# Optimization experiments

Hardware: AMD Instinct MI355X
Metric: run time of the kernel (lower is better)

Reference implementation:

```python
import jax, jax.numpy as jnp
import numpy as np

B, D, H, OUT = 1024, 1024, 16, 1000
DH = D // H          # 64 per-head dim
S = 50               # 49 patches + class token
EPS = 1e-5


def sinusoidal_pos_emb(seq_len, d_model):
    pos = jnp.arange(seq_len, dtype=jnp.float32)[:, None]
    i = jnp.arange(d_model, dtype=jnp.float32)[None, :]
    even = jnp.sin(pos / jnp.power(10000.0, i / d_model))
    odd = jnp.cos(pos / jnp.power(10000.0, (i - 1.0) / d_model))
    return jnp.where((jnp.arange(d_model) % 2 == 0)[None, :], even, odd)


def layernorm(x, w, b):
    mu = jnp.mean(x, axis=-1, keepdims=True)
    var = jnp.mean(jnp.square(x - mu), axis=-1, keepdims=True)
    return (x - mu) / jnp.sqrt(var + EPS) * w + b


def setup_inputs() -> dict:
    key = jax.random.key(0)
    ks = jax.random.split(key, 16)
    s = 1.0 / np.sqrt(DH)
    return {
        "x": jax.random.normal(ks[0], (B, 1, 28, 28), dtype=jnp.float32),
        "cls_token": jax.random.normal(ks[1], (1, D), dtype=jnp.float32),
        "Wp": jax.random.normal(ks[2], (D, 16), dtype=jnp.float32) * 0.25,
        "ln1_w": jnp.ones((D,), jnp.float32),
        "ln1_b": jnp.zeros((D,), jnp.float32),
        "Wq": jax.random.uniform(ks[3], (H, DH, DH), jnp.float32, -s, s),
        "bq": jax.random.uniform(ks[4], (H, DH), jnp.float32, -s, s),
        "Wk": jax.random.uniform(ks[5], (H, DH, DH), jnp.float32, -s, s),
        "bk": jax.random.uniform(ks[6], (H, DH), jnp.float32, -s, s),
        "Wv": jax.random.uniform(ks[7], (H, DH, DH), jnp.float32, -s, s),
        "bv": jax.random.uniform(ks[8], (H, DH), jnp.float32, -s, s),
        "ln2_w": jnp.ones((D,), jnp.float32),
        "ln2_b": jnp.zeros((D,), jnp.float32),
        "Wm": jax.random.normal(ks[9], (D, D), jnp.float32) / np.sqrt(D),
        "bm": jnp.zeros((D,), jnp.float32),
        "Wh": jax.random.normal(ks[10], (OUT, D), jnp.float32) / np.sqrt(D),
        "bh": jnp.zeros((OUT,), jnp.float32),
    }


def reference(x, cls_token, Wp, ln1_w, ln1_b, Wq, bq, Wk, bk, Wv, bv,
              ln2_w, ln2_b, Wm, bm, Wh, bh):
    b = x.shape[0]
    # patchify: (B,1,28,28) -> (B,49,16)  (7x7 patches of 4x4)
    p = x.reshape(b, 1, 7, 4, 7, 4).transpose(0, 1, 2, 4, 3, 5).reshape(b, 49, 16)
    tok = jnp.einsum('bps,ds->bpd', p, Wp)               # (B,49,D), no bias
    tok = jnp.concatenate([jnp.broadcast_to(cls_token[None], (b, 1, D)), tok], axis=1)
    tok = tok + sinusoidal_pos_emb(S, D)[None]           # (B,50,D)

    # transformer block (faithful: scores scaled by sqrt(d_model), full D)
    n = layernorm(tok, ln1_w, ln1_b)
    xh = n.reshape(b, S, H, DH).transpose(0, 2, 1, 3)    # (B,H,S,DH)
    q = jnp.einsum('bhsd,hed->bhse', xh, Wq) + bq[None, :, None, :]
    k = jnp.einsum('bhsd,hed->bhse', xh, Wk) + bk[None, :, None, :]
    v = jnp.einsum('bhsd,hed->bhse', xh, Wv) + bv[None, :, None, :]
    scores = jax.nn.softmax(jnp.einsum('bhqd,bhkd->bhqk', q, k) * jnp.sqrt(jnp.float32(D)), axis=-1)
    attn = jnp.einsum('bhqk,bhkd->bhqd', scores, v)      # (B,H,S,DH)
    A = attn.transpose(0, 2, 1, 3).reshape(b, S, D)
    tok = tok + A
    tok = tok + layernorm(tok, ln2_w, ln2_b) @ Wm.T + bm

    # classification head on class token
    logits = tok[:, 0] @ Wh.T + bh
    return jax.nn.softmax(logits, axis=-1)
```

## Files before the change

kernel.cpp:

```cpp
#include <hip/hip_runtime.h>
#include <math.h>


#define EPS 1e-5f

__device__ __forceinline__ float warp_sum64(float v) {
    #pragma unroll
    for (int off = 32; off >= 1; off >>= 1) v += __shfl_xor(v, off, 64);
    return v;
}
__device__ __forceinline__ float warp_max64(float v) {
    #pragma unroll
    for (int off = 32; off >= 1; off >>= 1) v = fmaxf(v, __shfl_xor(v, off, 64));
    return v;
}

__device__ __forceinline__ float block_sum(float v, float* red) {
    v = warp_sum64(v);
    int lane = threadIdx.x & 63, w = threadIdx.x >> 6;
    if (lane == 0) red[w] = v;
    __syncthreads();
    int nw = blockDim.x >> 6;
    if (w == 0) {
        float x = (lane < nw) ? red[lane] : 0.f;
        x = warp_sum64(x);
        if (lane == 0) red[0] = x;
    }
    __syncthreads();
    float r = red[0];
    __syncthreads();
    return r;
}

__device__ __forceinline__ float block_max(float v, float* red) {
    v = warp_max64(v);
    int lane = threadIdx.x & 63, w = threadIdx.x >> 6;
    if (lane == 0) red[w] = v;
    __syncthreads();
    int nw = blockDim.x >> 6;
    if (w == 0) {
        float x = (lane < nw) ? red[lane] : -INFINITY;
        x = warp_max64(x);
        if (lane == 0) red[0] = x;
    }
    __syncthreads();
    float r = red[0];
    __syncthreads();
    return r;
}

__global__ __launch_bounds__(256) void k_pe(float* __restrict__ pe) {
    int s = blockIdx.x;
    for (int d = threadIdx.x; d < 1024; d += 256) {
        int di = d & ~1;
        float freq = expf(-((float)di * (1.0f / 1024.f)) * 9.210340371976184f);
        float arg = (float)s * freq;
        pe[s * 1024 + d] = (d & 1) ? cosf(arg) : sinf(arg);
    }
}

__global__ __launch_bounds__(256) void k_prep_a(
    const float* __restrict__ cls, const float* __restrict__ pe,
    const float* __restrict__ ln1w, const float* __restrict__ ln1b,
    const float* __restrict__ Wq, const float* __restrict__ bq,
    const float* __restrict__ Wk,
    float* __restrict__ tok0c, float* __restrict__ n0g,
    float* __restrict__ qlw,
    float* __restrict__ score0, float* __restrict__ kap, float* __restrict__ bet)
{
    __shared__ float red[8];
    __shared__ float n0s[1024], q0s[1024];
    __shared__ float partA[256], partK[256], partB[256];
    int t = threadIdx.x;
    int h = t >> 4;

    float tv[4];
    #pragma unroll
    for (int i = 0; i < 4; ++i) {
        int d = t * 4 + i;
        tv[i] = cls[d] + pe[d];
        tok0c[d] = tv[i];
    }
    float sum = block_sum(tv[0] + tv[1] + tv[2] + tv[3], red);
    float mu = sum * (1.f / 1024.f);
    float d2 = 0.f;
    #pragma unroll
    for (int i = 0; i < 4; ++i) { float dv = tv[i] - mu; d2 = fmaf(dv, dv, d2); }
    float var = block_sum(d2, red) * (1.f / 1024.f);
    float rstd = rsqrtf(var + EPS);
    #pragma unroll
    for (int i = 0; i < 4; ++i) {
        int d = t * 4 + i;
        float nv = (tv[i] - mu) * rstd * ln1w[d] + ln1b[d];
        n0s[d] = nv; n0g[d] = nv;
    }
    __syncthreads();

    #pragma unroll
    for (int i = 0; i < 4; ++i) {
        int e = t * 4 + i, el = e & 63;
        const float* wr = Wq + ((size_t)h << 12) + el * 64;
        float acc = bq[e];
        for (int dd = 0; dd < 64; ++dd) acc = fmaf(wr[dd], n0s[(h << 6) + dd], acc);
        q0s[e] = acc;
    }
    __syncthreads();

    float pA = 0.f, pK = 0.f, pB = 0.f;
    #pragma unroll
    for (int i = 0; i < 4; ++i) {
        int d = t * 4 + i, dl = d & 63;
        const float* wc = Wk + ((size_t)h << 12) + dl;
        float acc = 0.f;
        for (int ee = 0; ee < 64; ++ee) acc = fmaf(wc[ee * 64], q0s[(h << 6) + ee], acc);
        acc *= 32.0f;
        float ql = acc * ln1w[d];
        qlw[d] = ql;
        pA = fmaf(acc, n0s[d], pA);
        pK += ql;
        pB = fmaf(acc, ln1b[d], pB);
    }
    partA[t] = pA; partK[t] = pK; partB[t] = pB;
    __syncthreads();
    if (t < 16) {
        float sA = 0.f, sK = 0.f, sB = 0.f;
        #pragma unroll
        for (int i = 0; i < 16; ++i) {
            sA += partA[t * 16 + i]; sK += partK[t * 16 + i]; sB += partB[t * 16 + i];
        }
        score0[t] = sA; kap[t] = sK; bet[t] = sB;
    }
}

__global__ __launch_bounds__(256) void k_prep_b(
    const float* __restrict__ pe, const float* __restrict__ Wp,
    const float* __restrict__ qlw,
    float* __restrict__ pwt, float* __restrict__ pe2t,
    float* __restrict__ pemean, float* __restrict__ pesum,
    float* __restrict__ Gt, float* __restrict__ ut, float* __restrict__ gt)
{
    int blk = blockIdx.x, t = threadIdx.x;
    if (blk < 50) {
        __shared__ float red[8];
        __shared__ float pwbuf[256 * 16];
        __shared__ float psbuf[256];
        int s = blk;
        float pwp[16];
        #pragma unroll
        for (int j = 0; j < 16; ++j) pwp[j] = 0.f;
        float pep = 0.f, pe2p = 0.f, psp = 0.f;
        #pragma unroll
        for (int i = 0; i < 4; ++i) {
            int d = t * 4 + i;
            float e = pe[s * 1024 + d];
            pep += e; pe2p = fmaf(e, e, pe2p); psp = fmaf(qlw[d], e, psp);
            const float* wr = Wp + (size_t)d * 16;
            #pragma unroll
            for (int j = 0; j < 16; ++j) pwp[j] = fmaf(wr[j], e, pwp[j]);
        }
        #pragma unroll
        for (int j = 0; j < 16; ++j) pwbuf[t * 16 + j] = pwp[j];
        psbuf[t] = psp;
        float pes = block_sum(pep, red);
        float pe2s = block_sum(pe2p, red);
        if (t < 16) {
            float a = 0.f;
            for (int k = 0; k < 256; ++k) a += pwbuf[k * 16 + t];
            pwt[s * 16 + t] = a;
            float b = 0.f;
            #pragma unroll
            for (int k = 0; k < 16; ++k) b += psbuf[t * 16 + k];
            pesum[s * 16 + t] = b;
        }
        if (t == 0) { pe2t[s] = pe2s; pemean[s] = pes * (1.f / 1024.f); }
    } else if (blk == 50) {
        int j = t >> 4, k = t & 15;
        float a = 0.f;
        for (int d = 0; d < 1024; ++d)
            a = fmaf(Wp[(size_t)d * 16 + j], Wp[(size_t)d * 16 + k], a);
        Gt[j * 16 + k] = a;
        if (t < 16) {
            float ua = 0.f;
            for (int d = 0; d < 1024; ++d) ua += Wp[(size_t)d * 16 + t];
            ut[t] = ua * (1.f / 1024.f);
        }
    } else {
        int h = t >> 4, j = t & 15;
        float a = 0.f;
        for (int dl = 0; dl < 64; ++dl) {
            int d = h * 64 + dl;
            a = fmaf(qlw[d], Wp[(size_t)d * 16 + j], a);
        }
        gt[h * 16 + j] = a;
    }
}

__global__ __launch_bounds__(256) void k_fused(
    const float* __restrict__ x, const float* __restrict__ pe,
    const float* __restrict__ Wp,
    const float* __restrict__ ln1w, const float* __restrict__ ln1b,
    const float* __restrict__ Wv, const float* __restrict__ bv,
    const float* __restrict__ n0g, const float* __restrict__ score0,
    const float* __restrict__ kap, const float* __restrict__ bet,
    const float* __restrict__ Gt, const float* __restrict__ ut,
    const float* __restrict__ gt,
    const float* __restrict__ pwt, const float* __restrict__ pe2t,
    const float* __restrict__ pemean, const float* __restrict__ pesum,
    float* __restrict__ A0)
{
    __shared__ float Gs[256], gs[256];
    __shared__ float us[16], kaps[16], bets[16], s0s[16];
    __shared__ int   prc[50];
    __shared__ float xs[4][800];
    __shared__ float mus[4][52], rss[4][52];
    __shared__ float sc[4][16][52];
    __shared__ float wpat[4][16][17];
    __shared__ float wmus[4][16];
    __shared__ float csh[4][16][68];

    int t = threadIdx.x, w = t >> 6, lane = t & 63;
    int b = blockIdx.x * 4 + w;

    Gs[t] = Gt[t];
    gs[t] = gt[t];
    if (t < 16) { us[t] = ut[t]; kaps[t] = kap[t]; bets[t] = bet[t]; s0s[t] = score0[t]; }
    if (t >= 1 && t < 50) prc[t] = ((t - 1) / 7) * 112 + ((t - 1) % 7) * 4;
    for (int i = lane; i < 784; i += 64) xs[w][i] = x[b * 784 + i];
    __syncthreads();

    {
        int s = lane;
        if (s >= 1 && s < 50) {
            float p[16];
            int off = prc[s];
            #pragma unroll
            for (int j = 0; j < 16; ++j) p[j] = xs[w][off + (j >> 2) * 28 + (j & 3)];
            float mu = pemean[s];
            #pragma unroll
            for (int j = 0; j < 16; ++j) mu = fmaf(us[j], p[j], mu);
            float ssq = pe2t[s];
            #pragma unroll
            for (int j = 0; j < 16; ++j) {
                float gpj = 0.f;
                #pragma unroll
                for (int k = 0; k < 16; ++k) gpj = fmaf(Gs[j * 16 + k], p[k], gpj);
                ssq = fmaf(p[j], gpj, ssq);
            }
            const float* pwr = pwt + s * 16;
            #pragma unroll
            for (int j = 0; j < 16; ++j) ssq = fmaf(2.f * p[j], pwr[j], ssq);
            float var = ssq * (1.f / 1024.f) - mu * mu;
            float rsv = rsqrtf(var + EPS);
            mus[w][s] = mu; rss[w][s] = rsv;
            const float* pss = pesum + s * 16;
            #pragma unroll
            for (int h = 0; h < 16; ++h) {
                float gp = 0.f;
                #pragma unroll
                for (int j = 0; j < 16; ++j) gp = fmaf(gs[h * 16 + j], p[j], gp);
                sc[w][h][s] = rsv * (gp + pss[h] - mu * kaps[h]) + bets[h];
            }
        } else if (s == 50) {
            #pragma unroll
            for (int h = 0; h < 16; ++h) sc[w][h][0] = s0s[h];
        }
    }
    __syncthreads();

    int h = lane & 15, q = lane >> 4;
    {
        int sb = q * 13, se = (sb + 13 < 50) ? sb + 13 : 50;
        float mx = -1e30f;
        for (int ss = sb; ss < se; ++ss) mx = fmaxf(mx, sc[w][h][ss]);
        mx = fmaxf(mx, __shfl_xor(mx, 16, 64));
        mx = fmaxf(mx, __shfl_xor(mx, 32, 64));
        float sm = 0.f;
        for (int ss = sb; ss < se; ++ss) {
            float e = expf(sc[w][h][ss] - mx);
            sc[w][h][ss] = e;
            sm += e;
        }
        sm += __shfl_xor(sm, 16, 64);
        sm += __shfl_xor(sm, 32, 64);
        float inv = 1.f / sm;
        for (int ss = sb; ss < se; ++ss) sc[w][h][ss] *= inv;
    }
    __syncthreads();

    {
        int sb = q * 13, se = (sb + 13 < 50) ? sb + 13 : 50;
        int s0c = (q == 0) ? 1 : sb;
        float acc[16], amu = 0.f;
        #pragma unroll
        for (int j = 0; j < 16; ++j) acc[j] = 0.f;
        for (int ss = s0c; ss < se; ++ss) {
            float wgt = sc[w][h][ss] * rss[w][ss];
            int off = prc[ss];
            #pragma unroll
            for (int j = 0; j < 16; ++j)
                acc[j] = fmaf(wgt, xs[w][off + (j >> 2) * 28 + (j & 3)], acc[j]);
            amu = fmaf(wgt, mus[w][ss], amu);
        }
        #pragma unroll
        for (int j = 0; j < 16; ++j) {
            acc[j] += __shfl_xor(acc[j], 16, 64);
            acc[j] += __shfl_xor(acc[j], 32, 64);
        }
        amu += __shfl_xor(amu, 16, 64);
        amu += __shfl_xor(amu, 32, 64);
        if (q == 0) {
            #pragma unroll
            for (int j = 0; j < 16; ++j) wpat[w][h][j] = acc[j];
            wmus[w][h] = amu;
        }
    }
    __syncthreads();

    {
        int d0 = lane * 16;
        int hh = lane >> 2;
        int dl0 = (lane & 3) * 16;
        float p0 = sc[w][hh][0];
        float wpe[16];
        #pragma unroll
        for (int i = 0; i < 16; ++i) wpe[i] = 0.f;
        for (int ss = 1; ss < 50; ++ss) {
            float wgt = sc[w][hh][ss] * rss[w][ss];
            const float4* per = (const float4*)(pe + ss * 1024 + d0);
            #pragma unroll
            for (int i4 = 0; i4 < 4; ++i4) {
                float4 v = per[i4];
                wpe[i4 * 4 + 0] = fmaf(wgt, v.x, wpe[i4 * 4 + 0]);
                wpe[i4 * 4 + 1] = fmaf(wgt, v.y, wpe[i4 * 4 + 1]);
                wpe[i4 * 4 + 2] = fmaf(wgt, v.z, wpe[i4 * 4 + 2]);
                wpe[i4 * 4 + 3] = fmaf(wgt, v.w, wpe[i4 * 4 + 3]);
            }
        }
        float wmu = wmus[w][hh];
        #pragma unroll
        for (int i = 0; i < 16; ++i) {
            int d = d0 + i;
            const float* wr = Wp + (size_t)d * 16;
            float wp_ = 0.f;
            #pragma unroll
            for (int j = 0; j < 16; ++j) wp_ = fmaf(wr[j], wpat[w][hh][j], wp_);
            float ci = p0 * n0g[d] + ln1w[d] * (wp_ + wpe[i] - wmu)
                     + ln1b[d] * (1.f - p0);
            csh[w][hh][dl0 + i] = ci;
        }
    }
    __syncthreads();

    {
        int e0 = lane * 16;
        int hh = lane >> 2;
        int el0 = (lane & 3) * 16;
        #pragma unroll
        for (int i = 0; i < 16; ++i) {
            int e = e0 + i;
            const float* wr = Wv + ((size_t)hh << 12) + (el0 + i) * 64;
            float acc = bv[e];
            #pragma unroll 16
            for (int dd = 0; dd < 64; ++dd)
                acc = fmaf(wr[dd], csh[w][hh][dd], acc);
            A0[(size_t)b * 1024 + e] = acc;
        }
    }
}

__global__ __launch_bounds__(256) void k_c1(
    const float* __restrict__ tok0c, const float* __restrict__ A0,
    const float* __restrict__ w2, const float* __restrict__ b2,
    float* __restrict__ tok0, float* __restrict__ n2)
{
    int b = blockIdx.x, tid = threadIdx.x;
    __shared__ float red[8];
    float t[4];
    #pragma unroll
    for (int i = 0; i < 4; ++i) {
        int d = tid + (i << 8);
        t[i] = tok0c[d] + A0[(size_t)b * 1024 + d];
    }
    float sum = block_sum(t[0] + t[1] + t[2] + t[3], red);
    float mu = sum * (1.f / 1024.f);
    float d2 = 0.f;
    #pragma unroll
    for (int i = 0; i < 4; ++i) { float dv = t[i] - mu; d2 = fmaf(dv, dv, d2); }
    float var = block_sum(d2, red) * (1.f / 1024.f);
    float rstd = rsqrtf(var + EPS);
    #pragma unroll
    for (int i = 0; i < 4; ++i) {
        int d = tid + (i << 8);
        tok0[(size_t)b * 1024 + d] = t[i];
        n2[(size_t)b * 1024 + d] = (t[i] - mu) * rstd * w2[d] + b2[d];
    }
}

__global__ __launch_bounds__(256) void k_gemm_sk(
    const float* __restrict__ A, const float* __restrict__ Bw,
    float* __restrict__ Cp, int N, int K)
{
    __shared__ __align__(16) float As[32 * 68];
    __shared__ __align__(16) float Bs[32 * 68];
    int n0 = blockIdx.x * 64, m0 = blockIdx.y * 64;
    int kz = blockIdx.z;
    int tid = threadIdx.x;
    int mt = (tid & 15) * 4, nt = (tid >> 4) * 4;
    float acc[4][4] = {{0.f}};

    int kbeg = kz * 128;
    for (int k0 = kbeg; k0 < kbeg + 128; k0 += 32) {
        for (int idx = tid; idx < 64 * 32; idx += 256) {
            int kk = idx & 31, m = idx >> 5;
            As[kk * 68 + m] = A[(size_t)(m0 + m) * K + k0 + kk];
            float bvv = (n0 + m < N) ? Bw[(size_t)(n0 + m) * K + k0 + kk] : 0.f;
            Bs[kk * 68 + m] = bvv;
        }
        __syncthreads();
        #pragma unroll 8
        for (int kk = 0; kk < 32; ++kk) {
            float4 av = *(const float4*)&As[kk * 68 + mt];
            float4 bv = *(const float4*)&Bs[kk * 68 + nt];
            acc[0][0] = fmaf(av.x, bv.x, acc[0][0]);
            acc[0][1] = fmaf(av.x, bv.y, acc[0][1]);
            acc[0][2] = fmaf(av.x, bv.z, acc[0][2]);
            acc[0][3] = fmaf(av.x, bv.w, acc[0][3]);
            acc[1][0] = fmaf(av.y, bv.x, acc[1][0]);
            acc[1][1] = fmaf(av.y, bv.y, acc[1][1]);
            acc[1][2] = fmaf(av.y, bv.z, acc[1][2]);
            acc[1][3] = fmaf(av.y, bv.w, acc[1][3]);
            acc[2][0] = fmaf(av.z, bv.x, acc[2][0]);
            acc[2][1] = fmaf(av.z, bv.y, acc[2][1]);
            acc[2][2] = fmaf(av.z, bv.z, acc[2][2]);
            acc[2][3] = fmaf(av.z, bv.w, acc[2][3]);
            acc[3][0] = fmaf(av.w, bv.x, acc[3][0]);
            acc[3][1] = fmaf(av.w, bv.y, acc[3][1]);
            acc[3][2] = fmaf(av.w, bv.z, acc[3][2]);
            acc[3][3] = fmaf(av.w, bv.w, acc[3][3]);
        }
        __syncthreads();
    }

    float* cpb = Cp + (size_t)kz * ((size_t)1024 * N);
    #pragma unroll
    for (int i = 0; i < 4; ++i) {
        int r = m0 + mt + i;
        #pragma unroll
        for (int j = 0; j < 4; ++j) {
            int c = n0 + nt + j;
            if (c < N) cpb[(size_t)r * N + c] = acc[i][j];
        }
    }
}

__global__ __launch_bounds__(256) void k_reduce(
    const float* __restrict__ Cp, const float* __restrict__ bias,
    const float* __restrict__ res, float* __restrict__ C, int N)
{
    const int N4 = N >> 2;
    int e4 = blockIdx.x * 256 + threadIdx.x;
    if (e4 >= 1024 * N4) return;
    int r = e4 / N4;
    int c = (e4 - r * N4) << 2;
    size_t off = (size_t)r * N + c;
    const size_t slice = (size_t)1024 * N;
    float4 s = make_float4(0.f, 0.f, 0.f, 0.f);
    #pragma unroll
    for (int kz = 0; kz < 8; ++kz) {
        float4 v = *(const float4*)(Cp + kz * slice + off);
        s.x += v.x; s.y += v.y; s.z += v.z; s.w += v.w;
    }
    float4 bb = *(const float4*)(bias + c);
    s.x += bb.x; s.y += bb.y; s.z += bb.z; s.w += bb.w;
    if (res) {
        float4 rv = *(const float4*)(res + off);
        s.x += rv.x; s.y += rv.y; s.z += rv.z; s.w += rv.w;
    }
    *(float4*)(C + off) = s;
}

__global__ __launch_bounds__(256) void k_softmax(
    const float* __restrict__ logits, float* __restrict__ out)
{
    int b = blockIdx.x, tid = threadIdx.x;
    __shared__ float red[8];
    float v[4];
    #pragma unroll
    for (int i = 0; i < 4; ++i) {
        int idx = tid + (i << 8);
        v[i] = (idx < 1000) ? logits[(size_t)b * 1000 + idx] : -INFINITY;
    }
    float mx = fmaxf(fmaxf(v[0], v[1]), fmaxf(v[2], v[3]));
    mx = block_max(mx, red);
    float e[4]; float s = 0.f;
    #pragma unroll
    for (int i = 0; i < 4; ++i) {
        int idx = tid + (i << 8);
        e[i] = (idx < 1000) ? expf(v[i] - mx) : 0.f;
        s += e[i];
    }
    s = block_sum(s, red);
    float inv = 1.f / s;
    #pragma unroll
    for (int i = 0; i < 4; ++i) {
        int idx = tid + (i << 8);
        if (idx < 1000) out[(size_t)b * 1000 + idx] = e[i] * inv;
    }
}

extern "C" void kernel_launch(void* const* d_in, const int* in_sizes, int n_in,
                              void* d_out, int out_size, void* d_ws, size_t ws_size,
                              hipStream_t stream)
{
    const float* x    = (const float*)d_in[0];
    const float* cls  = (const float*)d_in[1];
    const float* Wp   = (const float*)d_in[2];
    const float* ln1w = (const float*)d_in[3];
    const float* ln1b = (const float*)d_in[4];
    const float* Wq   = (const float*)d_in[5];
    const float* bq   = (const float*)d_in[6];
    const float* Wk   = (const float*)d_in[7];
    const float* bk   = (const float*)d_in[8];
    const float* Wv   = (const float*)d_in[9];
    const float* bv   = (const float*)d_in[10];
    const float* ln2w = (const float*)d_in[11];
    const float* ln2b = (const float*)d_in[12];
    const float* Wm   = (const float*)d_in[13];
    const float* bm   = (const float*)d_in[14];
    const float* Wh   = (const float*)d_in[15];
    const float* bh   = (const float*)d_in[16];
    float* out = (float*)d_out;
    (void)bk;

    char* ws = (char*)d_ws;
    size_t off = 0;
    auto alloc = [&](size_t nfloats) -> float* {
        float* p = (float*)(ws + off);
        off += ((nfloats * 4 + 255) & ~(size_t)255);
        return p;
    };
    float* pe     = alloc(50 * 1024);
    float* tok0c  = alloc(1024);
    float* n0g    = alloc(1024);
    float* qlw    = alloc(1024);
    float* score0 = alloc(16);
    float* kap    = alloc(16);
    float* bet    = alloc(16);
    float* Gt     = alloc(256);
    float* ut     = alloc(16);
    float* gt     = alloc(256);
    float* pwt    = alloc(50 * 16);
    float* pe2t   = alloc(50);
    float* pemean = alloc(50);
    float* pesum  = alloc(50 * 16);
    float* A0     = alloc((size_t)1024 * 1024);
    float* tok0   = alloc((size_t)1024 * 1024);
    float* n2     = alloc((size_t)1024 * 1024);
    float* t2     = alloc((size_t)1024 * 1024);
    float* logits = alloc((size_t)1024 * 1000);
    float* Cp     = alloc((size_t)8 * 1024 * 1024);

    k_pe<<<50, 256, 0, stream>>>(pe);
    k_prep_a<<<1, 256, 0, stream>>>(cls, pe, ln1w, ln1b, Wq, bq, Wk,
                                    tok0c, n0g, qlw, score0, kap, bet);
    k_prep_b<<<52, 256, 0, stream>>>(pe, Wp, qlw, pwt, pe2t, pemean, pesum,
                                     Gt, ut, gt);
    k_fused<<<256, 256, 0, stream>>>(x, pe, Wp, ln1w, ln1b, Wv, bv,
                                     n0g, score0, kap, bet, Gt, ut, gt,
                                     pwt, pe2t, pemean, pesum, A0);

    k_c1<<<1024, 256, 0, stream>>>(tok0c, A0, ln2w, ln2b, tok0, n2);

    k_gemm_sk<<<dim3(16, 16, 8), 256, 0, stream>>>(n2, Wm, Cp, 1024, 1024);
    k_reduce<<<1024, 256, 0, stream>>>(Cp, bm, tok0, t2, 1024);

    k_gemm_sk<<<dim3(16, 16, 8), 256, 0, stream>>>(t2, Wh, Cp, 1000, 1024);
    k_reduce<<<1000, 256, 0, stream>>>(Cp, bh, nullptr, logits, 1000);

    k_softmax<<<1024, 256, 0, stream>>>(logits, out);
}
```

Measured before the change: 332.1 us.

## Split per-head V projection into tiled GEMM kernel and enlarge split-K GEMM tiles

Moves the per-sample Wv projection out of the fused kernel into a separate tiled kernel (k_av) that reuses each head's Wv tile across 64 batch rows, with the intermediate written to a global buffer. The fused kernel's coalescing is changed so lanes index d by lane stride, and ln/n0 vectors are staged in shared memory. The split-K GEMM goes from 64x64 tiles with a 4x4 per-thread block to 128x128 tiles with an 8x8 per-thread block, which raises register pressure and leaves only 512 blocks per launch. The split adds one launch and a 4 MB global round-trip in exchange for far less redundant Wv traffic.

```diff
diff --git a/kernel.cpp b/kernel.cpp
--- a/kernel.cpp
+++ b/kernel.cpp
@@ -199,24 +199,23 @@
     const float* __restrict__ x, const float* __restrict__ pe,
     const float* __restrict__ Wp,
     const float* __restrict__ ln1w, const float* __restrict__ ln1b,
-    const float* __restrict__ Wv, const float* __restrict__ bv,
     const float* __restrict__ n0g, const float* __restrict__ score0,
     const float* __restrict__ kap, const float* __restrict__ bet,
     const float* __restrict__ Gt, const float* __restrict__ ut,
     const float* __restrict__ gt,
     const float* __restrict__ pwt, const float* __restrict__ pe2t,
     const float* __restrict__ pemean, const float* __restrict__ pesum,
-    float* __restrict__ A0)
+    float* __restrict__ cg)
 {
     __shared__ float Gs[256], gs[256];
     __shared__ float us[16], kaps[16], bets[16], s0s[16];
     __shared__ int   prc[50];
+    __shared__ float n0s[1024], lws[1024], lbs[1024];
     __shared__ float xs[4][800];
     __shared__ float mus[4][52], rss[4][52];
     __shared__ float sc[4][16][52];
     __shared__ float wpat[4][16][17];
     __shared__ float wmus[4][16];
-    __shared__ float csh[4][16][68];
 
     int t = threadIdx.x, w = t >> 6, lane = t & 63;
     int b = blockIdx.x * 4 + w;
@@ -225,6 +224,11 @@
     gs[t] = gt[t];
     if (t < 16) { us[t] = ut[t]; kaps[t] = kap[t]; bets[t] = bet[t]; s0s[t] = score0[t]; }
     if (t >= 1 && t < 50) prc[t] = ((t - 1) / 7) * 112 + ((t - 1) % 7) * 4;
+    #pragma unroll
+    for (int i = 0; i < 4; ++i) {
+        int d = t + (i << 8);
+        n0s[d] = n0g[d]; lws[d] = ln1w[d]; lbs[d] = ln1b[d];
+    }
     for (int i = lane; i < 784; i += 64) xs[w][i] = x[b * 784 + i];
     __syncthreads();
 
@@ -317,53 +321,87 @@
     __syncthreads();
 
     {
-        int d0 = lane * 16;
-        int hh = lane >> 2;
-        int dl0 = (lane & 3) * 16;
-        float p0 = sc[w][hh][0];
         float wpe[16];
         #pragma unroll
         for (int i = 0; i < 16; ++i) wpe[i] = 0.f;
         for (int ss = 1; ss < 50; ++ss) {
-            float wgt = sc[w][hh][ss] * rss[w][ss];
-            const float4* per = (const float4*)(pe + ss * 1024 + d0);
-            #pragma unroll
-            for (int i4 = 0; i4 < 4; ++i4) {
-                float4 v = per[i4];
-                wpe[i4 * 4 + 0] = fmaf(wgt, v.x, wpe[i4 * 4 + 0]);
-                wpe[i4 * 4 + 1] = fmaf(wgt, v.y, wpe[i4 * 4 + 1]);
-                wpe[i4 * 4 + 2] = fmaf(wgt, v.z, wpe[i4 * 4 + 2]);
-                wpe[i4 * 4 + 3] = fmaf(wgt, v.w, wpe[i4 * 4 + 3]);
+            float rsv = rss[w][ss];
+            const float* per = pe + ss * 1024 + lane;
+            #pragma unroll
+            for (int i = 0; i < 16; ++i) {
+                float wgt = sc[w][i][ss] * rsv;
+                wpe[i] = fmaf(wgt, per[i * 64], wpe[i]);
             }
         }
-        float wmu = wmus[w][hh];
         #pragma unroll
         for (int i = 0; i < 16; ++i) {
-            int d = d0 + i;
-            const float* wr = Wp + (size_t)d * 16;
+            int d = i * 64 + lane;
+            float p0 = sc[w][i][0];
+            const float4* wr = (const float4*)(Wp + (size_t)d * 16);
+            float4 wa = wr[0], wb = wr[1], wc = wr[2], wd = wr[3];
+            const float* wp_h = wpat[w][i];
             float wp_ = 0.f;
-            #pragma unroll
-            for (int j = 0; j < 16; ++j) wp_ = fmaf(wr[j], wpat[w][hh][j], wp_);
-            float ci = p0 * n0g[d] + ln1w[d] * (wp_ + wpe[i] - wmu)
-                     + ln1b[d] * (1.f - p0);
-            csh[w][hh][dl0 + i] = ci;
-        }
-    }
-    __syncthreads();
-
-    {
-        int e0 = lane * 16;
-        int hh = lane >> 2;
-        int el0 = (lane & 3) * 16;
-        #pragma unroll
-        for (int i = 0; i < 16; ++i) {
-            int e = e0 + i;
-            const float* wr = Wv + ((size_t)hh << 12) + (el0 + i) * 64;
-            float acc = bv[e];
-            #pragma unroll 16
-            for (int dd = 0; dd < 64; ++dd)
-                acc = fmaf(wr[dd], csh[w][hh][dd], acc);
-            A0[(size_t)b * 1024 + e] = acc;
+            wp_ = fmaf(wa.x, wp_h[0], wp_);  wp_ = fmaf(wa.y, wp_h[1], wp_);
+            wp_ = fmaf(wa.z, wp_h[2], wp_);  wp_ = fmaf(wa.w, wp_h[3], wp_);
+            wp_ = fmaf(wb.x, wp_h[4], wp_);  wp_ = fmaf(wb.y, wp_h[5], wp_);
+            wp_ = fmaf(wb.z, wp_h[6], wp_);  wp_ = fmaf(wb.w, wp_h[7], wp_);
+            wp_ = fmaf(wc.x, wp_h[8], wp_);  wp_ = fmaf(wc.y, wp_h[9], wp_);
+            wp_ = fmaf(wc.z, wp_h[10], wp_); wp_ = fmaf(wc.w, wp_h[11], wp_);
+            wp_ = fmaf(wd.x, wp_h[12], wp_); wp_ = fmaf(wd.y, wp_h[13], wp_);
+            wp_ = fmaf(wd.z, wp_h[14], wp_); wp_ = fmaf(wd.w, wp_h[15], wp_);
+            float ci = p0 * n0s[d] + lws[d] * (wp_ + wpe[i] - wmus[w][i])
+                     + lbs[d] * (1.f - p0);
+            cg[(size_t)b * 1024 + d] = ci;
+        }
+    }
+}
+
+__global__ __launch_bounds__(256) void k_av(
+    const float* __restrict__ cg, const float* __restrict__ Wv,
+    const float* __restrict__ bv, float* __restrict__ A0)
+{
+    __shared__ __align__(16) float wvt[64 * 68];
+    __shared__ __align__(16) float cst[64 * 68];
+    int b0 = blockIdx.x * 64, hh = blockIdx.y;
+    int tid = threadIdx.x;
+
+    for (int idx = tid; idx < 4096; idx += 256) {
+        int row = idx >> 6, col = idx & 63;
+        wvt[col * 68 + row] = Wv[((size_t)hh << 12) + idx];
+        cst[col * 68 + row] = cg[(size_t)(b0 + row) * 1024 + (hh << 6) + col];
+    }
+    __syncthreads();
+
+    int bt = (tid & 15) * 4, et = (tid >> 4) * 4;
+    float acc[4][4] = {{0.f}};
+    #pragma unroll 8
+    for (int d = 0; d < 64; ++d) {
+        float4 cv = *(const float4*)&cst[d * 68 + bt];
+        float4 wv4 = *(const float4*)&wvt[d * 68 + et];
+        acc[0][0] = fmaf(cv.x, wv4.x, acc[0][0]);
+        acc[0][1] = fmaf(cv.x, wv4.y, acc[0][1]);
+        acc[0][2] = fmaf(cv.x, wv4.z, acc[0][2]);
+        acc[0][3] = fmaf(cv.x, wv4.w, acc[0][3]);
+        acc[1][0] = fmaf(cv.y, wv4.x, acc[1][0]);
+        acc[1][1] = fmaf(cv.y, wv4.y, acc[1][1]);
+        acc[1][2] = fmaf(cv.y, wv4.z, acc[1][2]);
+        acc[1][3] = fmaf(cv.y, wv4.w, acc[1][3]);
+        acc[2][0] = fmaf(cv.z, wv4.x, acc[2][0]);
+        acc[2][1] = fmaf(cv.z, wv4.y, acc[2][1]);
+        acc[2][2] = fmaf(cv.z, wv4.z, acc[2][2]);
+        acc[2][3] = fmaf(cv.z, wv4.w, acc[2][3]);
+        acc[3][0] = fmaf(cv.w, wv4.x, acc[3][0]);
+        acc[3][1] = fmaf(cv.w, wv4.y, acc[3][1]);
+        acc[3][2] = fmaf(cv.w, wv4.z, acc[3][2]);
+        acc[3][3] = fmaf(cv.w, wv4.w, acc[3][3]);
+    }
+    #pragma unroll
+    for (int i = 0; i < 4; ++i) {
+        int b = b0 + bt + i;
+        #pragma unroll
+        for (int j = 0; j < 4; ++j) {
+            int e = (hh << 6) + et + j;
+            A0[(size_t)b * 1024 + e] = acc[i][j] + bv[e];
         }
     }
 }
@@ -400,53 +438,46 @@
     const float* __restrict__ A, const float* __restrict__ Bw,
     float* __restrict__ Cp, int N, int K)
 {
-    __shared__ __align__(16) float As[32 * 68];
-    __shared__ __align__(16) float Bs[32 * 68];
-    int n0 = blockIdx.x * 64, m0 = blockIdx.y * 64;
+    __shared__ __align__(16) float As[32 * 132];
+    __shared__ __align__(16) float Bs[32 * 132];
+    int n0 = blockIdx.x * 128, m0 = blockIdx.y * 128;
     int kz = blockIdx.z;
     int tid = threadIdx.x;
-    int mt = (tid & 15) * 4, nt = (tid >> 4) * 4;
-    float acc[4][4] = {{0.f}};
+    int mt = (tid & 15) * 8, nt = (tid >> 4) * 8;
+    float acc[8][8] = {{0.f}};
 
     int kbeg = kz * 128;
     for (int k0 = kbeg; k0 < kbeg + 128; k0 += 32) {
-        for (int idx = tid; idx < 64 * 32; idx += 256) {
+        for (int idx = tid; idx < 128 * 32; idx += 256) {
             int kk = idx & 31, m = idx >> 5;
-            As[kk * 68 + m] = A[(size_t)(m0 + m) * K + k0 + kk];
+            As[kk * 132 + m] = A[(size_t)(m0 + m) * K + k0 + kk];
             float bvv = (n0 + m < N) ? Bw[(size_t)(n0 + m) * K + k0 + kk] : 0.f;
-            Bs[kk * 68 + m] = bvv;
+            Bs[kk * 132 + m] = bvv;
         }
         __syncthreads();
-        #pragma unroll 8
+        #pragma unroll 4
         for (int kk = 0; kk < 32; ++kk) {
-            float4 av = *(const float4*)&As[kk * 68 + mt];
-            float4 bv = *(const float4*)&Bs[kk * 68 + nt];
-            acc[0][0] = fmaf(av.x, bv.x, acc[0][0]);
-            acc[0][1] = fmaf(av.x, bv.y, acc[0][1]);
-            acc[0][2] = fmaf(av.x, bv.z, acc[0][2]);
-            acc[0][3] = fmaf(av.x, bv.w, acc[0][3]);
-            acc[1][0] = fmaf(av.y, bv.x, acc[1][0]);
-            acc[1][1] = fmaf(av.y, bv.y, acc[1][1]);
-            acc[1][2] = fmaf(av.y, bv.z, acc[1][2]);
-            acc[1][3] = fmaf(av.y, bv.w, acc[1][3]);
-            acc[2][0] = fmaf(av.z, bv.x, acc[2][0]);
-            acc[2][1] = fmaf(av.z, bv.y, acc[2][1]);
-            acc[2][2] = fmaf(av.z, bv.z, acc[2][2]);
-            acc[2][3] = fmaf(av.z, bv.w, acc[2][3]);
-            acc[3][0] = fmaf(av.w, bv.x, acc[3][0]);
-            acc[3][1] = fmaf(av.w, bv.y, acc[3][1]);
-            acc[3][2] = fmaf(av.w, bv.z, acc[3][2]);
-            acc[3][3] = fmaf(av.w, bv.w, acc[3][3]);
+            float4 a0 = *(const float4*)&As[kk * 132 + mt];
+            float4 a1 = *(const float4*)&As[kk * 132 + mt + 4];
+            float4 b0 = *(const float4*)&Bs[kk * 132 + nt];
+            float4 b1 = *(const float4*)&Bs[kk * 132 + nt + 4];
+            float av[8] = {a0.x, a0.y, a0.z, a0.w, a1.x, a1.y, a1.z, a1.w};
+            float bvr[8] = {b0.x, b0.y, b0.z, b0.w, b1.x, b1.y, b1.z, b1.w};
+            #pragma unroll
+            for (int i = 0; i < 8; ++i)
+                #pragma unroll
+                for (int j = 0; j < 8; ++j)
+                    acc[i][j] = fmaf(av[i], bvr[j], acc[i][j]);
         }
         __syncthreads();
     }
 
     float* cpb = Cp + (size_t)kz * ((size_t)1024 * N);
     #pragma unroll
-    for (int i = 0; i < 4; ++i) {
+    for (int i = 0; i < 8; ++i) {
         int r = m0 + mt + i;
         #pragma unroll
-        for (int j = 0; j < 4; ++j) {
+        for (int j = 0; j < 8; ++j) {
             int c = n0 + nt + j;
             if (c < N) cpb[(size_t)r * N + c] = acc[i][j];
         }
@@ -553,6 +584,7 @@
     float* pe2t   = alloc(50);
     float* pemean = alloc(50);
     float* pesum  = alloc(50 * 16);
+    float* cg     = alloc((size_t)1024 * 1024);
     float* A0     = alloc((size_t)1024 * 1024);
     float* tok0   = alloc((size_t)1024 * 1024);
     float* n2     = alloc((size_t)1024 * 1024);
@@ -565,16 +597,17 @@
                                     tok0c, n0g, qlw, score0, kap, bet);
     k_prep_b<<<52, 256, 0, stream>>>(pe, Wp, qlw, pwt, pe2t, pemean, pesum,
                                      Gt, ut, gt);
-    k_fused<<<256, 256, 0, stream>>>(x, pe, Wp, ln1w, ln1b, Wv, bv,
+    k_fused<<<256, 256, 0, stream>>>(x, pe, Wp, ln1w, ln1b,
                                      n0g, score0, kap, bet, Gt, ut, gt,
-                                     pwt, pe2t, pemean, pesum, A0);
+                                     pwt, pe2t, pemean, pesum, cg);
+    k_av<<<dim3(16, 16), 256, 0, stream>>>(cg, Wv, bv, A0);
 
     k_c1<<<1024, 256, 0, stream>>>(tok0c, A0, ln2w, ln2b, tok0, n2);
 
-    k_gemm_sk<<<dim3(16, 16, 8), 256, 0, stream>>>(n2, Wm, Cp, 1024, 1024);
+    k_gemm_sk<<<dim3(8, 8, 8), 256, 0, stream>>>(n2, Wm, Cp, 1024, 1024);
     k_reduce<<<1024, 256, 0, stream>>>(Cp, bm, tok0, t2, 1024);
 
-    k_gemm_sk<<<dim3(16, 16, 8), 256, 0, stream>>>(t2, Wh, Cp, 1000, 1024);
+    k_gemm_sk<<<dim3(8, 8, 8), 256, 0, stream>>>(t2, Wh, Cp, 1000, 1024);
     k_reduce<<<1000, 256, 0, stream>>>(Cp, bh, nullptr, logits, 1000);
 
     k_softmax<<<1024, 256, 0, stream>>>(logits, out);
```

Result: slower. 368.6 us (+11.0%).
